# Kernel tuning notes

Hardware: AMD Instinct MI355X
Metric: run time of the kernel (lower is better)

The kernel has to match this reference:

```python
import jax, jax.numpy as jnp
import numpy as np

B_SZ, SEQ, D_MODEL, N_STATE = 4, 2048, 768, 16


def setup_inputs() -> dict:
    key = jax.random.key(0)
    ks = jax.random.split(key, 8)
    s = 1.0 / np.sqrt(D_MODEL)
    x = jax.random.normal(ks[0], (B_SZ, SEQ, D_MODEL), dtype=jnp.float32)
    W1 = jax.random.uniform(ks[1], (D_MODEL, D_MODEL), jnp.float32, -s, s)
    b1 = jax.random.uniform(ks[2], (D_MODEL,), jnp.float32, -s, s)
    W2 = jax.random.uniform(ks[3], (D_MODEL, N_STATE), jnp.float32, -s, s)
    b2 = jax.random.uniform(ks[4], (N_STATE,), jnp.float32, -s, s)
    W3 = jax.random.uniform(ks[5], (D_MODEL, N_STATE), jnp.float32, -s, s)
    b3 = jax.random.uniform(ks[6], (N_STATE,), jnp.float32, -s, s)
    # A: xavier_uniform over (d_model, state_size)
    a_bound = np.sqrt(6.0 / (D_MODEL + N_STATE))
    A = jax.random.uniform(ks[7], (D_MODEL, N_STATE), jnp.float32, -a_bound, a_bound)
    return {"x": x, "W1": W1, "b1": b1, "W2": W2, "b2": b2, "W3": W3, "b3": b3, "A": A}


def reference(x, W1, b1, W2, b2, W3, b3, A):
    # Input-dependent projections
    Bm = x @ W2 + b2                     # [b, l, n]
    Cm = x @ W3 + b3                     # [b, l, n]
    delta = jax.nn.softplus(x @ W1 + b1)  # [b, l, d]
    # Discretization (S6)
    dB = delta[..., None] * Bm[:, :, None, :]                 # [b, l, d, n]
    dA = jnp.exp(jnp.einsum('bld,dn->bldn', delta, A))        # [b, l, d, n]
    # Source initializes h to zeros, so the dA*h term vanishes (no recurrence).
    h0 = jnp.zeros_like(dB)
    h = dA * h0 + x[..., None] * dB                            # [b, l, d, n]
    y = jnp.einsum('bln,bldn->bld', Cm, h)                     # [b, l, d]
    return y
```

## Files before the change

### kernel.cpp

```cpp
#include <hip/hip_runtime.h>
#include <hip/hip_bf16.h>
#include <math.h>


#define M_ROWS 8192
#define DM 768
#define NS 16

typedef short bf16x8 __attribute__((ext_vector_type(8)));
typedef float f32x4 __attribute__((ext_vector_type(4)));

__device__ __forceinline__ unsigned short f2bf(float f) {
    union { float f; unsigned u; } v; v.f = f;
    unsigned r = v.u + 0x7FFF + ((v.u >> 16) & 1);
    return (unsigned short)(r >> 16);
}
__device__ __forceinline__ float bf2f(unsigned short h) {
    union { unsigned u; float f; } v; v.u = ((unsigned)h) << 16; return v.f;
}
__device__ __forceinline__ void async16(const void* g, void* l) {
    __builtin_amdgcn_global_load_lds(
        (const __attribute__((address_space(1))) void*)g,
        (__attribute__((address_space(3))) void*)l,
        16, 0, 0);
}
__device__ __forceinline__ float softplus_fast(float v) {
    return fmaxf(v, 0.f) + __logf(1.f + __expf(-fabsf(v)));
}

__global__ __launch_bounds__(256) void prep_kernel(
    const float* __restrict__ x,
    const float* __restrict__ W1,
    const float* __restrict__ W2,
    const float* __restrict__ W3,
    unsigned short* __restrict__ xb,
    unsigned short* __restrict__ w1t,
    unsigned short* __restrict__ w23t)
{
    __shared__ float tile[32][33];
    const int bid = blockIdx.x;
    const int tid = threadIdx.x;
    if (bid < 32) {
        const int n = bid, i = n >> 1;
        const float* src = (n & 1) ? W3 : W2;
        #pragma unroll
        for (int e = 0; e < 3; ++e) {
            int k = e * 256 + tid;
            w23t[n * DM + k] = f2bf(src[k * NS + i]);
        }
    } else if (bid < 608) {
        const int b2i = bid - 32;
        const int n0 = (b2i % 24) * 32, k0 = (b2i / 24) * 32;
        const int tx = tid & 31, ty = tid >> 5;
        #pragma unroll
        for (int i = 0; i < 4; ++i) {
            int k = ty + i * 8;
            tile[k][tx] = W1[(k0 + k) * DM + n0 + tx];
        }
        __syncthreads();
        #pragma unroll
        for (int i = 0; i < 4; ++i) {
            int n = ty + i * 8;
            w1t[(n0 + n) * DM + k0 + tx] = f2bf(tile[tx][n]);
        }
    } else {
        int i = (bid - 608) * 256 + tid;
        float4 v = ((const float4*)x)[i];
        ushort4 o;
        o.x = f2bf(v.x); o.y = f2bf(v.y); o.z = f2bf(v.z); o.w = f2bf(v.w);
        ((ushort4*)xb)[i] = o;
    }
}

__global__ __launch_bounds__(256) void sgemm_kernel(
    const unsigned short* __restrict__ xb,
    const unsigned short* __restrict__ w23t,
    const float* __restrict__ b2, const float* __restrict__ b3,
    float* __restrict__ s_out)
{
    __shared__ unsigned short Al[64 * 64];
    __shared__ unsigned short Bl[32 * 64];
    const int m0 = blockIdx.x * 64;
    const int tid = threadIdx.x, lane = tid & 63, wave = tid >> 6;
    const int l15 = lane & 15, quad = lane >> 4;

    f32x4 acc[2];
    acc[0] = (f32x4){0.f,0.f,0.f,0.f};
    acc[1] = (f32x4){0.f,0.f,0.f,0.f};

    for (int k0 = 0; k0 < DM; k0 += 64) {
        #pragma unroll
        for (int i = 0; i < 2; ++i) {
            int ch = tid + i * 256;
            int r = ch >> 3, jg = (ch & 7) ^ (r & 7);
            async16(xb + (m0 + r) * DM + k0 + jg * 8, Al + ch * 8);
        }
        {
            int ch = tid;
            int r = ch >> 3, jg = (ch & 7) ^ (r & 7);
            async16(w23t + r * DM + k0 + jg * 8, Bl + ch * 8);
        }
        __syncthreads();
        #pragma unroll
        for (int kk = 0; kk < 2; ++kk) {
            int rr = wave * 16 + l15;
            int ja = (kk * 4 + quad) ^ (rr & 7);
            bf16x8 af = *(const bf16x8*)(Al + rr * 64 + ja * 8);
            #pragma unroll
            for (int t = 0; t < 2; ++t) {
                int rb = t * 16 + l15;
                int jb = (kk * 4 + quad) ^ (rb & 7);
                bf16x8 bfr = *(const bf16x8*)(Bl + rb * 64 + jb * 8);
                acc[t] = __builtin_amdgcn_mfma_f32_16x16x32_bf16(
                    af, bfr, acc[t], 0, 0, 0);
            }
        }
        __syncthreads();
    }

    float sacc[4] = {0.f, 0.f, 0.f, 0.f};
    #pragma unroll
    for (int t = 0; t < 2; ++t) {
        int p = t * 8 + (l15 >> 1);
        float bB = b2[p], bC = b3[p];
        #pragma unroll
        for (int r = 0; r < 4; ++r) {
            float v = acc[t][r];
            float pv = __shfl_xor(v, 1, 64);
            float term = (l15 & 1) ? (pv + bB) * (v + bC)
                                   : (v + bB) * (pv + bC);
            sacc[r] += term;
        }
    }
    #pragma unroll
    for (int r = 0; r < 4; ++r) {
        sacc[r] += __shfl_xor(sacc[r], 1, 64);
        sacc[r] += __shfl_xor(sacc[r], 2, 64);
        sacc[r] += __shfl_xor(sacc[r], 4, 64);
        sacc[r] += __shfl_xor(sacc[r], 8, 64);
    }
    if (l15 == 0) {
        #pragma unroll
        for (int r = 0; r < 4; ++r)
            s_out[m0 + wave * 16 + quad * 4 + r] = 0.5f * sacc[r];
    }
}

__global__ __launch_bounds__(256) void gemm_fused_kernel(
    const unsigned short* __restrict__ xb,
    const unsigned short* __restrict__ w1t,
    const float* __restrict__ b1,
    const float* __restrict__ s_arr,
    float* __restrict__ y)
{
    __shared__ unsigned short Al[128 * 64];
    __shared__ unsigned short Bl[64 * 64];
    const int b = blockIdx.x;
    const int c = b & 7, j = b >> 3;
    const int m0 = (c * 8 + j / 12) * 128;
    const int n0 = (j % 12) * 64;
    const int tid  = threadIdx.x;
    const int lane = tid & 63;
    const int wave = tid >> 6;
    const int wm = wave >> 1, wn = wave & 1;
    const int l15 = lane & 15, quad = lane >> 4;

    f32x4 acc[4][2];
    #pragma unroll
    for (int i = 0; i < 4; ++i)
        #pragma unroll
        for (int jj = 0; jj < 2; ++jj)
            acc[i][jj] = (f32x4){0.f, 0.f, 0.f, 0.f};

    for (int k0 = 0; k0 < DM; k0 += 64) {
        #pragma unroll
        for (int i = 0; i < 4; ++i) {
            int ch = tid + i * 256;
            int r = ch >> 3, jg = (ch & 7) ^ (r & 7);
            async16(xb + (m0 + r) * DM + k0 + jg * 8, Al + ch * 8);
        }
        #pragma unroll
        for (int i = 0; i < 2; ++i) {
            int ch = tid + i * 256;
            int r = ch >> 3, jg = (ch & 7) ^ (r & 7);
            async16(w1t + (n0 + r) * DM + k0 + jg * 8, Bl + ch * 8);
        }
        __syncthreads();

        #pragma unroll
        for (int kk = 0; kk < 2; ++kk) {
            bf16x8 bfr[2];
            #pragma unroll
            for (int jj = 0; jj < 2; ++jj) {
                int rb = wn * 32 + jj * 16 + l15;
                int jb = (kk * 4 + quad) ^ (rb & 7);
                bfr[jj] = *(const bf16x8*)(Bl + rb * 64 + jb * 8);
            }
            #pragma unroll
            for (int i = 0; i < 4; ++i) {
                int rr = wm * 64 + i * 16 + l15;
                int ja = (kk * 4 + quad) ^ (rr & 7);
                bf16x8 af = *(const bf16x8*)(Al + rr * 64 + ja * 8);
                #pragma unroll
                for (int jj = 0; jj < 2; ++jj)
                    acc[i][jj] = __builtin_amdgcn_mfma_f32_16x16x32_bf16(
                        af, bfr[jj], acc[i][jj], 0, 0, 0);
            }
        }
        __syncthreads();
    }

    #pragma unroll
    for (int i = 0; i < 4; ++i) {
        const int rowbase = m0 + wm * 64 + i * 16 + quad * 4;
        float4 s4 = *(const float4*)(s_arr + rowbase);
        #pragma unroll
        for (int jj = 0; jj < 2; ++jj) {
            int gcol = n0 + wn * 32 + jj * 16 + l15;
            float bias = b1[gcol];
            #pragma unroll
            for (int r = 0; r < 4; ++r) {
                int grow = rowbase + r;
                float v = acc[i][jj][r] + bias;
                float sp = softplus_fast(v);
                float xv = bf2f(xb[grow * DM + gcol]);
                float sv = (r == 0) ? s4.x : (r == 1) ? s4.y : (r == 2) ? s4.z : s4.w;
                y[grow * DM + gcol] = xv * sp * sv;
            }
        }
    }
}

extern "C" void kernel_launch(void* const* d_in, const int* in_sizes, int n_in,
                              void* d_out, int out_size, void* d_ws, size_t ws_size,
                              hipStream_t stream) {
    const float* x  = (const float*)d_in[0];
    const float* W1 = (const float*)d_in[1];
    const float* b1 = (const float*)d_in[2];
    const float* W2 = (const float*)d_in[3];
    const float* b2 = (const float*)d_in[4];
    const float* W3 = (const float*)d_in[5];
    const float* b3 = (const float*)d_in[6];
    float* y = (float*)d_out;

    unsigned short* xb   = (unsigned short*)d_ws;
    unsigned short* w1t  = (unsigned short*)((char*)d_ws + 12582912);
    unsigned short* w23t = (unsigned short*)((char*)d_ws + 13762560);
    float*          sarr = (float*)((char*)d_ws + 13811712);

    prep_kernel<<<6752, 256, 0, stream>>>(x, W1, W2, W3, xb, w1t, w23t);
    sgemm_kernel<<<128, 256, 0, stream>>>(xb, w23t, b2, b3, sarr);
    gemm_fused_kernel<<<768, 256, 0, stream>>>(xb, w1t, b1, sarr, y);
}
```

Measured before the change: 116.4 us.

## Load GEMM MFMA fragments directly from global memory with register double buffering

The main fused GEMM no longer stages x and W1 tiles through LDS with async loads and barriers. Each lane now loads its bf16 MFMA fragments straight from global memory into registers, using two register sets so the next K-step's loads overlap the current MFMAs. This removes LDS traffic and the per-step __syncthreads. In exchange, operand reuse across waves now depends on L1/L2 caching, global loads become strided per row, and register pressure rises.

```diff
diff --git a/kernel.cpp b/kernel.cpp
--- a/kernel.cpp
+++ b/kernel.cpp
@@ -153,18 +153,18 @@
     const float* __restrict__ s_arr,
     float* __restrict__ y)
 {
-    __shared__ unsigned short Al[128 * 64];
-    __shared__ unsigned short Bl[64 * 64];
     const int b = blockIdx.x;
     const int c = b & 7, j = b >> 3;
     const int m0 = (c * 8 + j / 12) * 128;
     const int n0 = (j % 12) * 64;
-    const int tid  = threadIdx.x;
-    const int lane = tid & 63;
-    const int wave = tid >> 6;
+    const int lane = threadIdx.x & 63;
+    const int wave = threadIdx.x >> 6;
     const int wm = wave >> 1, wn = wave & 1;
     const int l15 = lane & 15, quad = lane >> 4;
 
+    const unsigned short* Abase = xb  + (size_t)(m0 + wm * 64 + l15) * DM + quad * 8;
+    const unsigned short* Bbase = w1t + (size_t)(n0 + wn * 32 + l15) * DM + quad * 8;
+
     f32x4 acc[4][2];
     #pragma unroll
     for (int i = 0; i < 4; ++i)
@@ -172,43 +172,38 @@
         for (int jj = 0; jj < 2; ++jj)
             acc[i][jj] = (f32x4){0.f, 0.f, 0.f, 0.f};
 
-    for (int k0 = 0; k0 < DM; k0 += 64) {
-        #pragma unroll
-        for (int i = 0; i < 4; ++i) {
-            int ch = tid + i * 256;
-            int r = ch >> 3, jg = (ch & 7) ^ (r & 7);
-            async16(xb + (m0 + r) * DM + k0 + jg * 8, Al + ch * 8);
-        }
-        #pragma unroll
-        for (int i = 0; i < 2; ++i) {
-            int ch = tid + i * 256;
-            int r = ch >> 3, jg = (ch & 7) ^ (r & 7);
-            async16(w1t + (n0 + r) * DM + k0 + jg * 8, Bl + ch * 8);
-        }
-        __syncthreads();
-
-        #pragma unroll
-        for (int kk = 0; kk < 2; ++kk) {
-            bf16x8 bfr[2];
-            #pragma unroll
-            for (int jj = 0; jj < 2; ++jj) {
-                int rb = wn * 32 + jj * 16 + l15;
-                int jb = (kk * 4 + quad) ^ (rb & 7);
-                bfr[jj] = *(const bf16x8*)(Bl + rb * 64 + jb * 8);
-            }
-            #pragma unroll
-            for (int i = 0; i < 4; ++i) {
-                int rr = wm * 64 + i * 16 + l15;
-                int ja = (kk * 4 + quad) ^ (rr & 7);
-                bf16x8 af = *(const bf16x8*)(Al + rr * 64 + ja * 8);
-                #pragma unroll
-                for (int jj = 0; jj < 2; ++jj)
-                    acc[i][jj] = __builtin_amdgcn_mfma_f32_16x16x32_bf16(
-                        af, bfr[jj], acc[i][jj], 0, 0, 0);
-            }
-        }
-        __syncthreads();
-    }
+#define LOAD_FRAGS(da, db, koff)                                              \
+    {                                                                         \
+        _Pragma("unroll") for (int i = 0; i < 4; ++i)                         \
+            _Pragma("unroll") for (int kk = 0; kk < 2; ++kk)                  \
+                da[i][kk] = *(const bf16x8*)(Abase + (size_t)i * 16 * DM      \
+                                             + (koff) + kk * 32);             \
+        _Pragma("unroll") for (int jj = 0; jj < 2; ++jj)                      \
+            _Pragma("unroll") for (int kk = 0; kk < 2; ++kk)                  \
+                db[jj][kk] = *(const bf16x8*)(Bbase + (size_t)jj * 16 * DM    \
+                                              + (koff) + kk * 32);            \
+    }
+#define DO_MFMA(sa, sb)                                                       \
+    {                                                                         \
+        _Pragma("unroll") for (int kk = 0; kk < 2; ++kk)                      \
+            _Pragma("unroll") for (int i = 0; i < 4; ++i)                     \
+                _Pragma("unroll") for (int jj = 0; jj < 2; ++jj)              \
+                    acc[i][jj] = __builtin_amdgcn_mfma_f32_16x16x32_bf16(     \
+                        sa[i][kk], sb[jj][kk], acc[i][jj], 0, 0, 0);          \
+    }
+
+    bf16x8 aA[4][2], bA[2][2], aB[4][2], bB[2][2];
+    LOAD_FRAGS(aA, bA, 0);
+    #pragma unroll
+    for (int s2 = 0; s2 < 6; ++s2) {
+        LOAD_FRAGS(aB, bB, (2 * s2 + 1) * 64);
+        DO_MFMA(aA, bA);
+        if (s2 < 5)
+            LOAD_FRAGS(aA, bA, (2 * s2 + 2) * 64);
+        DO_MFMA(aB, bB);
+    }
+#undef LOAD_FRAGS
+#undef DO_MFMA
 
     #pragma unroll
     for (int i = 0; i < 4; ++i) {
```

Measured after the change: 152.1 us. 1.31x slower.

## Fuse the B/C projection dot-product into the main W1 GEMM kernel

Applied to the files above, without the earlier changes.

Removes the separate sgemm kernel that computed per-row s = sum(Bm*Cm) and instead computes it inside the main GEMM. Each block also loads the 32x768 W2/W3 tile and runs extra MFMAs, then reduces through shared memory. This drops one launch and the global round trip for s. In exchange, every one of the 768 blocks recomputes the projection for its 128 rows (12x redundancy across column tiles) and holds more registers and LDS.

```diff
diff --git a/kernel.cpp b/kernel.cpp
--- a/kernel.cpp
+++ b/kernel.cpp
@@ -72,89 +72,18 @@
     }
 }
 
-__global__ __launch_bounds__(256) void sgemm_kernel(
-    const unsigned short* __restrict__ xb,
-    const unsigned short* __restrict__ w23t,
-    const float* __restrict__ b2, const float* __restrict__ b3,
-    float* __restrict__ s_out)
-{
-    __shared__ unsigned short Al[64 * 64];
-    __shared__ unsigned short Bl[32 * 64];
-    const int m0 = blockIdx.x * 64;
-    const int tid = threadIdx.x, lane = tid & 63, wave = tid >> 6;
-    const int l15 = lane & 15, quad = lane >> 4;
-
-    f32x4 acc[2];
-    acc[0] = (f32x4){0.f,0.f,0.f,0.f};
-    acc[1] = (f32x4){0.f,0.f,0.f,0.f};
-
-    for (int k0 = 0; k0 < DM; k0 += 64) {
-        #pragma unroll
-        for (int i = 0; i < 2; ++i) {
-            int ch = tid + i * 256;
-            int r = ch >> 3, jg = (ch & 7) ^ (r & 7);
-            async16(xb + (m0 + r) * DM + k0 + jg * 8, Al + ch * 8);
-        }
-        {
-            int ch = tid;
-            int r = ch >> 3, jg = (ch & 7) ^ (r & 7);
-            async16(w23t + r * DM + k0 + jg * 8, Bl + ch * 8);
-        }
-        __syncthreads();
-        #pragma unroll
-        for (int kk = 0; kk < 2; ++kk) {
-            int rr = wave * 16 + l15;
-            int ja = (kk * 4 + quad) ^ (rr & 7);
-            bf16x8 af = *(const bf16x8*)(Al + rr * 64 + ja * 8);
-            #pragma unroll
-            for (int t = 0; t < 2; ++t) {
-                int rb = t * 16 + l15;
-                int jb = (kk * 4 + quad) ^ (rb & 7);
-                bf16x8 bfr = *(const bf16x8*)(Bl + rb * 64 + jb * 8);
-                acc[t] = __builtin_amdgcn_mfma_f32_16x16x32_bf16(
-                    af, bfr, acc[t], 0, 0, 0);
-            }
-        }
-        __syncthreads();
-    }
-
-    float sacc[4] = {0.f, 0.f, 0.f, 0.f};
-    #pragma unroll
-    for (int t = 0; t < 2; ++t) {
-        int p = t * 8 + (l15 >> 1);
-        float bB = b2[p], bC = b3[p];
-        #pragma unroll
-        for (int r = 0; r < 4; ++r) {
-            float v = acc[t][r];
-            float pv = __shfl_xor(v, 1, 64);
-            float term = (l15 & 1) ? (pv + bB) * (v + bC)
-                                   : (v + bB) * (pv + bC);
-            sacc[r] += term;
-        }
-    }
-    #pragma unroll
-    for (int r = 0; r < 4; ++r) {
-        sacc[r] += __shfl_xor(sacc[r], 1, 64);
-        sacc[r] += __shfl_xor(sacc[r], 2, 64);
-        sacc[r] += __shfl_xor(sacc[r], 4, 64);
-        sacc[r] += __shfl_xor(sacc[r], 8, 64);
-    }
-    if (l15 == 0) {
-        #pragma unroll
-        for (int r = 0; r < 4; ++r)
-            s_out[m0 + wave * 16 + quad * 4 + r] = 0.5f * sacc[r];
-    }
-}
-
 __global__ __launch_bounds__(256) void gemm_fused_kernel(
     const unsigned short* __restrict__ xb,
     const unsigned short* __restrict__ w1t,
+    const unsigned short* __restrict__ w23t,
     const float* __restrict__ b1,
-    const float* __restrict__ s_arr,
+    const float* __restrict__ b2, const float* __restrict__ b3,
     float* __restrict__ y)
 {
     __shared__ unsigned short Al[128 * 64];
     __shared__ unsigned short Bl[64 * 64];
+    __shared__ unsigned short Wl[32 * 64];
+    __shared__ float spart[2][128];
     const int b = blockIdx.x;
     const int c = b & 7, j = b >> 3;
     const int m0 = (c * 8 + j / 12) * 128;
@@ -166,11 +95,14 @@
     const int l15 = lane & 15, quad = lane >> 4;
 
     f32x4 acc[4][2];
+    f32x4 accP[4];
     #pragma unroll
-    for (int i = 0; i < 4; ++i)
+    for (int i = 0; i < 4; ++i) {
+        accP[i] = (f32x4){0.f, 0.f, 0.f, 0.f};
         #pragma unroll
         for (int jj = 0; jj < 2; ++jj)
             acc[i][jj] = (f32x4){0.f, 0.f, 0.f, 0.f};
+    }
 
     for (int k0 = 0; k0 < DM; k0 += 64) {
         #pragma unroll
@@ -185,16 +117,26 @@
             int r = ch >> 3, jg = (ch & 7) ^ (r & 7);
             async16(w1t + (n0 + r) * DM + k0 + jg * 8, Bl + ch * 8);
         }
+        {
+            int ch = tid;
+            int r = ch >> 3, jg = (ch & 7) ^ (r & 7);
+            async16(w23t + r * DM + k0 + jg * 8, Wl + ch * 8);
+        }
         __syncthreads();
 
         #pragma unroll
         for (int kk = 0; kk < 2; ++kk) {
-            bf16x8 bfr[2];
+            bf16x8 bfr[2], wfr;
             #pragma unroll
             for (int jj = 0; jj < 2; ++jj) {
                 int rb = wn * 32 + jj * 16 + l15;
                 int jb = (kk * 4 + quad) ^ (rb & 7);
                 bfr[jj] = *(const bf16x8*)(Bl + rb * 64 + jb * 8);
+            }
+            {
+                int rw = wn * 16 + l15;
+                int jw = (kk * 4 + quad) ^ (rw & 7);
+                wfr = *(const bf16x8*)(Wl + rw * 64 + jw * 8);
             }
             #pragma unroll
             for (int i = 0; i < 4; ++i) {
@@ -205,15 +147,47 @@
                 for (int jj = 0; jj < 2; ++jj)
                     acc[i][jj] = __builtin_amdgcn_mfma_f32_16x16x32_bf16(
                         af, bfr[jj], acc[i][jj], 0, 0, 0);
+                accP[i] = __builtin_amdgcn_mfma_f32_16x16x32_bf16(
+                    af, wfr, accP[i], 0, 0, 0);
             }
         }
         __syncthreads();
     }
+
+    {
+        const int p = wn * 8 + (l15 >> 1);
+        const float bB = b2[p], bC = b3[p];
+        #pragma unroll
+        for (int i = 0; i < 4; ++i) {
+            float sacc[4];
+            #pragma unroll
+            for (int r = 0; r < 4; ++r) {
+                float v = accP[i][r];
+                float pv = __shfl_xor(v, 1, 64);
+                sacc[r] = (l15 & 1) ? (pv + bB) * (v + bC)
+                                    : (v + bB) * (pv + bC);
+                sacc[r] += __shfl_xor(sacc[r], 1, 64);
+                sacc[r] += __shfl_xor(sacc[r], 2, 64);
+                sacc[r] += __shfl_xor(sacc[r], 4, 64);
+                sacc[r] += __shfl_xor(sacc[r], 8, 64);
+            }
+            if (l15 == 0) {
+                #pragma unroll
+                for (int r = 0; r < 4; ++r)
+                    spart[wn][wm * 64 + i * 16 + quad * 4 + r] = 0.5f * sacc[r];
+            }
+        }
+    }
+    __syncthreads();
 
     #pragma unroll
     for (int i = 0; i < 4; ++i) {
-        const int rowbase = m0 + wm * 64 + i * 16 + quad * 4;
-        float4 s4 = *(const float4*)(s_arr + rowbase);
+        const int rl = wm * 64 + i * 16 + quad * 4;
+        const int rowbase = m0 + rl;
+        float sv4[4];
+        #pragma unroll
+        for (int r = 0; r < 4; ++r)
+            sv4[r] = spart[0][rl + r] + spart[1][rl + r];
         #pragma unroll
         for (int jj = 0; jj < 2; ++jj) {
             int gcol = n0 + wn * 32 + jj * 16 + l15;
@@ -224,8 +198,7 @@
                 float v = acc[i][jj][r] + bias;
                 float sp = softplus_fast(v);
                 float xv = bf2f(xb[grow * DM + gcol]);
-                float sv = (r == 0) ? s4.x : (r == 1) ? s4.y : (r == 2) ? s4.z : s4.w;
-                y[grow * DM + gcol] = xv * sp * sv;
+                y[grow * DM + gcol] = xv * sp * sv4[r];
             }
         }
     }
@@ -246,9 +219,7 @@
     unsigned short* xb   = (unsigned short*)d_ws;
     unsigned short* w1t  = (unsigned short*)((char*)d_ws + 12582912);
     unsigned short* w23t = (unsigned short*)((char*)d_ws + 13762560);
-    float*          sarr = (float*)((char*)d_ws + 13811712);
 
     prep_kernel<<<6752, 256, 0, stream>>>(x, W1, W2, W3, xb, w1t, w23t);
-    sgemm_kernel<<<128, 256, 0, stream>>>(xb, w23t, b2, b3, sarr);
-    gemm_fused_kernel<<<768, 256, 0, stream>>>(xb, w1t, b1, sarr, y);
-}
+    gemm_fused_kernel<<<768, 256, 0, stream>>>(xb, w1t, w23t, b1, b2, b3, y);
+}
```

New measurement: 112.1 us. 3.6% less time.
